# Kernel optimization log

Hardware: AMD Instinct MI355X
Metric: run time of the kernel (lower is better)

## Reference

```python
import jax, jax.numpy as jnp
import numpy as np

N = 6144          # nodes
F_IN = 512        # num_feature
HID = 64          # hidden_dim
C = 40            # num_class
H = 3             # num_heads
ALPHA = 0.2       # leaky relu slope
NEG_INF = -9e15


def gat_layer(x, adj, W, a_src, a_dst):
    # x: [N, f_in], W: [H, f_in, f_out], a_src/a_dst: [H, f_out]
    Wh = jnp.einsum('nf,hfo->hno', x, W)                  # [H, N, f_out]
    e_src = jnp.einsum('hno,ho->hn', Wh, a_src)           # [H, N]
    e_dst = jnp.einsum('hno,ho->hn', Wh, a_dst)           # [H, N]
    e = jax.nn.leaky_relu(e_src[:, :, None] + e_dst[:, None, :], ALPHA)  # [H, N, N]
    scores = jnp.where(adj > 0, e, NEG_INF)               # mask non-edges
    attn = jax.nn.softmax(scores, axis=-1)                # softmax over neighbors
    out = jnp.einsum('hnm,hmo->hno', attn, Wh)            # [H, N, f_out]
    return out.mean(axis=0)                               # average heads -> [N, f_out]


def setup_inputs() -> dict:
    key = jax.random.key(0)
    k = jax.random.split(key, 8)
    feature = jax.random.normal(k[0], (N, F_IN), dtype=jnp.float32)
    adj = (jax.random.uniform(k[1], (N, N)) < 0.01).astype(jnp.float32)
    adj = jnp.maximum(adj, jnp.eye(N, dtype=jnp.float32))
    s1 = 1.0 / np.sqrt(F_IN)
    s2 = 1.0 / np.sqrt(HID)
    W1 = jax.random.normal(k[2], (H, F_IN, HID), dtype=jnp.float32) * s1
    a1_src = jax.random.normal(k[3], (H, HID), dtype=jnp.float32) * s2
    a1_dst = jax.random.normal(k[4], (H, HID), dtype=jnp.float32) * s2
    W2 = jax.random.normal(k[5], (H, HID, C), dtype=jnp.float32) * s2
    a2_src = jax.random.normal(k[6], (H, C), dtype=jnp.float32) * (1.0 / np.sqrt(C))
    a2_dst = jax.random.normal(k[7], (H, C), dtype=jnp.float32) * (1.0 / np.sqrt(C))
    return {"feature": feature, "adj": adj, "W1": W1, "a1_src": a1_src,
            "a1_dst": a1_dst, "W2": W2, "a2_src": a2_src, "a2_dst": a2_dst}


def reference(feature, adj, W1, a1_src, a1_dst, W2, a2_src, a2_dst):
    # eval mode: dropout is identity
    x = jax.nn.relu(gat_layer(feature, adj, W1, a1_src, a1_dst))  # [N, HID]
    x = gat_layer(x, adj, W2, a2_src, a2_dst)                     # [N, C]
    return jax.nn.log_softmax(x, axis=1)
```

## Files before the change

### kernel.cpp

```cpp
#include <hip/hip_runtime.h>
#include <math.h>

#define NN   6144
#define FIN  512
#define HIDN 64
#define NC   40
#define NH   3
#define CAP  128
#define NCHUNK (CAP / 64)
#define LALPHA 0.2f
#define KSPLIT 4
#define PK_LOW  0x3FFFu
#define PK_HIGH 0xFFFFC000u

__device__ __forceinline__ float bf2f(ushort s) {
    return __uint_as_float((unsigned)s << 16);
}
__device__ __forceinline__ ushort f2bf(float f) {
    unsigned u = __float_as_uint(f);
    return (ushort)((u + 0x7FFFu + ((u >> 16) & 1u)) >> 16);
}

__global__ __launch_bounds__(256) void k_csr(const float* __restrict__ adj,
                                             int* __restrict__ nbr,
                                             int* __restrict__ deg) {
    int row  = blockIdx.x * 4 + (threadIdx.x >> 6);
    int lane = threadIdx.x & 63;
    const float* arow = adj + (size_t)row * NN;
    int* nrow = nbr + (size_t)row * CAP;
    int cnt = 0;

    float4 cur[4], nxt[4];
#pragma unroll
    for (int i = 0; i < 4; i++)
        cur[i] = *reinterpret_cast<const float4*>(arow + i * 256 + lane * 4);

#pragma unroll
    for (int g = 0; g < 6; g++) {
        if (g < 5) {
#pragma unroll
            for (int i = 0; i < 4; i++)
                nxt[i] = *reinterpret_cast<const float4*>(arow + (g + 1) * 1024 + i * 256 + lane * 4);
        }
#pragma unroll
        for (int i = 0; i < 4; i++) {
            int base = g * 1024 + i * 256;
            float vv[4] = {cur[i].x, cur[i].y, cur[i].z, cur[i].w};
#pragma unroll
            for (int q = 0; q < 4; q++) {
                bool on = vv[q] > 0.0f;
                unsigned long long mask = __ballot(on);
                if (on) {
                    int pos = cnt + __popcll(mask & ((1ull << lane) - 1ull));
                    if (pos < CAP) nrow[pos] = base + lane * 4 + q;
                }
                cnt += __popcll(mask);
            }
        }
#pragma unroll
        for (int i = 0; i < 4; i++) cur[i] = nxt[i];
    }
    if (lane == 0) deg[row] = cnt < CAP ? cnt : CAP;
}

__global__ __launch_bounds__(256) void k_gemm1(const float* __restrict__ x,
                                               const float* __restrict__ W,
                                               float* __restrict__ Whp) {
    __shared__ float xs[64][68];
    __shared__ float wsh[64][68];
    int h  = blockIdx.y;
    int n0 = blockIdx.x * 64;
    int kz = blockIdx.z;
    int tid = threadIdx.x;
    int og4 = (tid & 15) * 4;
    int mg4 = (tid >> 4) * 4;

    float acc[4][4] = {{0.f}};

    const float* xbase0 = x + (size_t)n0 * FIN;
    const float* wbase0 = W + (size_t)h * FIN * HIDN;

    for (int t = 0; t < 2; t++) {
        int k0 = kz * 128 + t * 64;
#pragma unroll
        for (int i = 0; i < 4; i++) {
            int l = tid + i * 256;
            int r = l >> 4;
            int c = (l & 15) * 4;
            *reinterpret_cast<float4*>(&xs[r][c]) =
                *reinterpret_cast<const float4*>(xbase0 + (size_t)r * FIN + k0 + c);
            *reinterpret_cast<float4*>(&wsh[r][c]) =
                *reinterpret_cast<const float4*>(wbase0 + (size_t)(k0 + r) * HIDN + c);
        }
        __syncthreads();

#pragma unroll 8
        for (int k = 0; k < 64; k += 4) {
            float4 xv[4], wv[4];
            xv[0] = *reinterpret_cast<const float4*>(&xs[mg4 + 0][k]);
            xv[1] = *reinterpret_cast<const float4*>(&xs[mg4 + 1][k]);
            xv[2] = *reinterpret_cast<const float4*>(&xs[mg4 + 2][k]);
            xv[3] = *reinterpret_cast<const float4*>(&xs[mg4 + 3][k]);
            wv[0] = *reinterpret_cast<const float4*>(&wsh[k + 0][og4]);
            wv[1] = *reinterpret_cast<const float4*>(&wsh[k + 1][og4]);
            wv[2] = *reinterpret_cast<const float4*>(&wsh[k + 2][og4]);
            wv[3] = *reinterpret_cast<const float4*>(&wsh[k + 3][og4]);
            const float* xf = reinterpret_cast<const float*>(xv);
            const float* wf = reinterpret_cast<const float*>(wv);
#pragma unroll
            for (int i = 0; i < 4; i++) {
#pragma unroll
                for (int kk = 0; kk < 4; kk++) {
                    float xval = xf[i * 4 + kk];
#pragma unroll
                    for (int j = 0; j < 4; j++)
                        acc[i][j] += xval * wf[kk * 4 + j];
                }
            }
        }
        __syncthreads();
    }

    float* outp = Whp + (((size_t)kz * NH + h) * NN + n0 + mg4) * HIDN + og4;
#pragma unroll
    for (int i = 0; i < 4; i++) {
        float4 v = make_float4(acc[i][0], acc[i][1], acc[i][2], acc[i][3]);
        *reinterpret_cast<float4*>(outp + (size_t)i * HIDN) = v;
    }
}

__global__ __launch_bounds__(256) void k_sum_e1(const float* __restrict__ Whp,
                                                const float* __restrict__ a_src,
                                                const float* __restrict__ a_dst,
                                                ushort* __restrict__ Whb,
                                                float* __restrict__ es,
                                                float* __restrict__ ed) {
    int gw   = blockIdx.x * 4 + (threadIdx.x >> 6);
    int lane = threadIdx.x & 63;
    int h = gw / NN, n = gw % NN;
    size_t idx = ((size_t)h * NN + n) * HIDN + lane;
    size_t stride = (size_t)NH * NN * HIDN;
    float v = Whp[idx] + Whp[idx + stride] + Whp[idx + 2 * stride] + Whp[idx + 3 * stride];
    Whb[idx] = f2bf(v);
    float s = v * a_src[h * HIDN + lane];
    float d = v * a_dst[h * HIDN + lane];
#pragma unroll
    for (int off = 32; off; off >>= 1) {
        s += __shfl_xor(s, off);
        d += __shfl_xor(d, off);
    }
    if (lane == 0) { es[h * NN + n] = s; ed[h * NN + n] = d; }
}

__global__ __launch_bounds__(192) void k_attn1f(const int* __restrict__ nbr,
                                                const int* __restrict__ deg,
                                                const ushort* __restrict__ Whb,
                                                const float* __restrict__ es,
                                                const float* __restrict__ ed,
                                                const float* __restrict__ W2,
                                                const float* __restrict__ a2s,
                                                const float* __restrict__ a2d,
                                                ushort* __restrict__ Wh2b,
                                                float* __restrict__ e2s,
                                                float* __restrict__ e2d) {
    __shared__ unsigned pks[NH][CAP];
    __shared__ float hsum[NH][HIDN];
    int n = blockIdx.x;
    int h = threadIdx.x >> 6;
    int lane = threadIdx.x & 63;
    int d = deg[n];
    const int* nrow = nbr + (size_t)n * CAP;
    float esv = es[h * NN + n];

    float psum = 0.f;
#pragma unroll
    for (int c = 0; c < NCHUNK; c++) {
        int k = c * 64 + lane;
        unsigned u = 0;
        if (k < d) {
            int mm = nrow[k];
            float e = esv + ed[h * NN + mm];
            float s = e > 0.f ? e : LALPHA * e;
            float p = __expf(s);
            u = (__float_as_uint(p) & PK_HIGH) | (unsigned)mm;
            psum += __uint_as_float(u & PK_HIGH);
        }
        pks[h][k] = u;
    }
#pragma unroll
    for (int off = 32; off; off >>= 1) psum += __shfl_xor(psum, off);
    float inv = 1.f / psum;
    __syncthreads();

    const ushort* WhH = Whb + (size_t)h * NN * HIDN + lane;
    float a0 = 0.f, a1 = 0.f, a2 = 0.f, a3 = 0.f;
    int iters = (d + 3) >> 2;
    for (int g = 0; g < iters; g++) {
        uint4 uu = *reinterpret_cast<const uint4*>(&pks[h][g * 4]);
        a0 += __uint_as_float(uu.x & PK_HIGH) * bf2f(WhH[(size_t)(uu.x & PK_LOW) * HIDN]);
        a1 += __uint_as_float(uu.y & PK_HIGH) * bf2f(WhH[(size_t)(uu.y & PK_LOW) * HIDN]);
        a2 += __uint_as_float(uu.z & PK_HIGH) * bf2f(WhH[(size_t)(uu.z & PK_LOW) * HIDN]);
        a3 += __uint_as_float(uu.w & PK_HIGH) * bf2f(WhH[(size_t)(uu.w & PK_LOW) * HIDN]);
    }
    float hacc = ((a0 + a1) + (a2 + a3));
    hsum[h][lane] = hacc * inv;
    __syncthreads();

    float xv = (hsum[0][lane] + hsum[1][lane] + hsum[2][lane]) * (1.f / NH);
    xv = fmaxf(xv, 0.f);

    int c = lane < NC ? lane : NC - 1;
    float acc = 0.f;
#pragma unroll 8
    for (int o = 0; o < HIDN; o++) {
        float xb = __shfl(xv, o);
        float wv = W2[((size_t)h * HIDN + o) * NC + c];
        acc += xb * wv;
    }
    if (lane >= NC) acc = 0.f;

    float s2 = acc * (lane < NC ? a2s[h * NC + lane] : 0.f);
    float d2 = acc * (lane < NC ? a2d[h * NC + lane] : 0.f);
#pragma unroll
    for (int off = 32; off; off >>= 1) {
        s2 += __shfl_xor(s2, off);
        d2 += __shfl_xor(d2, off);
    }
    if (lane < NC) Wh2b[((size_t)h * NN + n) * NC + lane] = f2bf(acc);
    if (lane == 0) { e2s[h * NN + n] = s2; e2d[h * NN + n] = d2; }
}

__global__ __launch_bounds__(192) void k_attn2(const int* __restrict__ nbr,
                                               const int* __restrict__ deg,
                                               const ushort* __restrict__ Wh2b,
                                               const float* __restrict__ es,
                                               const float* __restrict__ ed,
                                               float* __restrict__ out) {
    __shared__ unsigned pks[NH][CAP];
    __shared__ float hsum[NH][HIDN];
    int n = blockIdx.x;
    int h = threadIdx.x >> 6;
    int lane = threadIdx.x & 63;
    int d = deg[n];
    const int* nrow = nbr + (size_t)n * CAP;
    float esv = es[h * NN + n];

    float psum = 0.f;
#pragma unroll
    for (int c = 0; c < NCHUNK; c++) {
        int k = c * 64 + lane;
        unsigned u = 0;
        if (k < d) {
            int mm = nrow[k];
            float e = esv + ed[h * NN + mm];
            float s = e > 0.f ? e : LALPHA * e;
            float p = __expf(s);
            u = (__float_as_uint(p) & PK_HIGH) | (unsigned)mm;
            psum += __uint_as_float(u & PK_HIGH);
        }
        pks[h][k] = u;
    }
#pragma unroll
    for (int off = 32; off; off >>= 1) psum += __shfl_xor(psum, off);
    float inv = 1.f / psum;
    __syncthreads();

    const ushort* W2H = Wh2b + (size_t)h * NN * NC + (lane < NC ? lane : 0);
    float a0 = 0.f, a1 = 0.f, a2 = 0.f, a3 = 0.f;
    int iters = (d + 3) >> 2;
    for (int g = 0; g < iters; g++) {
        uint4 uu = *reinterpret_cast<const uint4*>(&pks[h][g * 4]);
        a0 += __uint_as_float(uu.x & PK_HIGH) * bf2f(W2H[(size_t)(uu.x & PK_LOW) * NC]);
        a1 += __uint_as_float(uu.y & PK_HIGH) * bf2f(W2H[(size_t)(uu.y & PK_LOW) * NC]);
        a2 += __uint_as_float(uu.z & PK_HIGH) * bf2f(W2H[(size_t)(uu.z & PK_LOW) * NC]);
        a3 += __uint_as_float(uu.w & PK_HIGH) * bf2f(W2H[(size_t)(uu.w & PK_LOW) * NC]);
    }
    float hacc = ((a0 + a1) + (a2 + a3));
    if (lane < NC) hsum[h][lane] = hacc * inv;
    __syncthreads();

    if (threadIdx.x < 64) {
        float a = (lane < NC)
            ? (hsum[0][lane] + hsum[1][lane] + hsum[2][lane]) * (1.f / NH)
            : -INFINITY;
        float mx = a;
#pragma unroll
        for (int off = 32; off; off >>= 1) mx = fmaxf(mx, __shfl_xor(mx, off));
        float ex = (lane < NC) ? __expf(a - mx) : 0.f;
        float se = ex;
#pragma unroll
        for (int off = 32; off; off >>= 1) se += __shfl_xor(se, off);
        if (lane < NC) out[(size_t)n * NC + lane] = a - mx - logf(se);
    }
}

extern "C" void kernel_launch(void* const* d_in, const int* in_sizes, int n_in,
                              void* d_out, int out_size, void* d_ws, size_t ws_size,
                              hipStream_t stream) {
    const float* feature = (const float*)d_in[0];
    const float* adj     = (const float*)d_in[1];
    const float* W1      = (const float*)d_in[2];
    const float* a1_src  = (const float*)d_in[3];
    const float* a1_dst  = (const float*)d_in[4];
    const float* W2      = (const float*)d_in[5];
    const float* a2_src  = (const float*)d_in[6];
    const float* a2_dst  = (const float*)d_in[7];
    float* out = (float*)d_out;

    char* ws = (char*)d_ws;
    size_t off = 0;
    int*    nbr = (int*)(ws + off);    off += (size_t)NN * CAP * sizeof(int);
    int*    deg = (int*)(ws + off);    off += (size_t)NN * sizeof(int);
    float*  Whp = (float*)(ws + off);  off += (size_t)KSPLIT * NH * NN * HIDN * sizeof(float);
    ushort* Whb = (ushort*)(ws + off); off += (size_t)NH * NN * HIDN * sizeof(ushort);
    float*  e1s = (float*)(ws + off);  off += (size_t)NH * NN * sizeof(float);
    float*  e1d = (float*)(ws + off);  off += (size_t)NH * NN * sizeof(float);
    ushort* Wh2b= (ushort*)(ws + off); off += (size_t)NH * NN * NC * sizeof(ushort);
    float*  e2s = (float*)(ws + off);  off += (size_t)NH * NN * sizeof(float);
    float*  e2d = (float*)(ws + off);  off += (size_t)NH * NN * sizeof(float);

    k_csr<<<NN / 4, 256, 0, stream>>>(adj, nbr, deg);
    k_gemm1<<<dim3(NN / 64, NH, KSPLIT), 256, 0, stream>>>(feature, W1, Whp);
    k_sum_e1<<<(NH * NN) / 4, 256, 0, stream>>>(Whp, a1_src, a1_dst, Whb, e1s, e1d);
    k_attn1f<<<NN, 192, 0, stream>>>(nbr, deg, Whb, e1s, e1d, W2, a2_src, a2_dst,
                                     Wh2b, e2s, e2d);
    k_attn2<<<NN, 192, 0, stream>>>(nbr, deg, Wh2b, e2s, e2d, out);
}
```

Measured before the change: 103.5 us.

## Split adjacency CSR build into bitmask pass and fused compaction with head sum

```diff
diff --git a/kernel.cpp b/kernel.cpp
--- a/kernel.cpp
+++ b/kernel.cpp
@@ -12,6 +12,11 @@
 #define KSPLIT 4
 #define PK_LOW  0x3FFFu
 #define PK_HIGH 0xFFFFC000u
+#define NGRP   (NN * NN / 256)
+#define BITS_WAVES 8192
+#define CSRB   (NN / 4)
+
+typedef unsigned long long ull;
 
 __device__ __forceinline__ float bf2f(ushort s) {
     return __uint_as_float((unsigned)s << 16);
@@ -21,46 +26,26 @@
     return (ushort)((u + 0x7FFFu + ((u >> 16) & 1u)) >> 16);
 }
 
-__global__ __launch_bounds__(256) void k_csr(const float* __restrict__ adj,
-                                             int* __restrict__ nbr,
-                                             int* __restrict__ deg) {
-    int row  = blockIdx.x * 4 + (threadIdx.x >> 6);
+__global__ __launch_bounds__(256) void k_bits(const float* __restrict__ adj,
+                                              ull* __restrict__ bits) {
+    int gwid = (blockIdx.x * 256 + (int)threadIdx.x) >> 6;
     int lane = threadIdx.x & 63;
-    const float* arow = adj + (size_t)row * NN;
-    int* nrow = nbr + (size_t)row * CAP;
-    int cnt = 0;
-
-    float4 cur[4], nxt[4];
-#pragma unroll
-    for (int i = 0; i < 4; i++)
-        cur[i] = *reinterpret_cast<const float4*>(arow + i * 256 + lane * 4);
-
-#pragma unroll
-    for (int g = 0; g < 6; g++) {
-        if (g < 5) {
-#pragma unroll
-            for (int i = 0; i < 4; i++)
-                nxt[i] = *reinterpret_cast<const float4*>(arow + (g + 1) * 1024 + i * 256 + lane * 4);
-        }
-#pragma unroll
-        for (int i = 0; i < 4; i++) {
-            int base = g * 1024 + i * 256;
-            float vv[4] = {cur[i].x, cur[i].y, cur[i].z, cur[i].w};
-#pragma unroll
-            for (int q = 0; q < 4; q++) {
-                bool on = vv[q] > 0.0f;
-                unsigned long long mask = __ballot(on);
-                if (on) {
-                    int pos = cnt + __popcll(mask & ((1ull << lane) - 1ull));
-                    if (pos < CAP) nrow[pos] = base + lane * 4 + q;
-                }
-                cnt += __popcll(mask);
-            }
-        }
-#pragma unroll
-        for (int i = 0; i < 4; i++) cur[i] = nxt[i];
-    }
-    if (lane == 0) deg[row] = cnt < CAP ? cnt : CAP;
+#pragma unroll 2
+    for (int it = 0; it < NGRP / BITS_WAVES; it++) {
+        size_t grp = (size_t)it * BITS_WAVES + gwid;
+        const float* p = adj + grp * 256 + lane;
+        float a0 = p[0], a1 = p[64], a2 = p[128], a3 = p[192];
+        ull m0 = __ballot(a0 > 0.f);
+        ull m1 = __ballot(a1 > 0.f);
+        ull m2 = __ballot(a2 > 0.f);
+        ull m3 = __ballot(a3 > 0.f);
+        if (lane == 0) {
+            ulonglong2* q = reinterpret_cast<ulonglong2*>(bits + grp * 4);
+            ulonglong2 v0; v0.x = m0; v0.y = m1;
+            ulonglong2 v1; v1.x = m2; v1.y = m3;
+            q[0] = v0; q[1] = v1;
+        }
+    }
 }
 
 __global__ __launch_bounds__(256) void k_gemm1(const float* __restrict__ x,
@@ -76,7 +61,6 @@
     int mg4 = (tid >> 4) * 4;
 
     float acc[4][4] = {{0.f}};
-
     const float* xbase0 = x + (size_t)n0 * FIN;
     const float* wbase0 = W + (size_t)h * FIN * HIDN;
 
@@ -129,14 +113,52 @@
     }
 }
 
-__global__ __launch_bounds__(256) void k_sum_e1(const float* __restrict__ Whp,
-                                                const float* __restrict__ a_src,
-                                                const float* __restrict__ a_dst,
-                                                ushort* __restrict__ Whb,
-                                                float* __restrict__ es,
-                                                float* __restrict__ ed) {
-    int gw   = blockIdx.x * 4 + (threadIdx.x >> 6);
+__global__ __launch_bounds__(256) void k_csr2_sume1(const ull* __restrict__ bits,
+                                                    int* __restrict__ nbr,
+                                                    int* __restrict__ deg,
+                                                    const float* __restrict__ Whp,
+                                                    const float* __restrict__ a_src,
+                                                    const float* __restrict__ a_dst,
+                                                    ushort* __restrict__ Whb,
+                                                    float* __restrict__ es,
+                                                    float* __restrict__ ed) {
     int lane = threadIdx.x & 63;
+    if (blockIdx.x < CSRB) {
+        int row = blockIdx.x * 4 + ((int)threadIdx.x >> 6);
+        const ull* brow = bits + (size_t)row * 96;
+        ull m0 = brow[lane];
+        ull m1 = (lane < 32) ? brow[64 + lane] : 0ull;
+        int c0 = __popcll(m0), c1 = __popcll(m1);
+        int s0 = c0, s1 = c1;
+#pragma unroll
+        for (int off = 1; off < 64; off <<= 1) {
+            int t0 = __shfl_up(s0, off);
+            int t1 = __shfl_up(s1, off);
+            if (lane >= off) { s0 += t0; s1 += t1; }
+        }
+        int total0 = __shfl(s0, 63);
+        int total  = total0 + __shfl(s1, 63);
+        int pre0 = s0 - c0;
+        int pre1 = total0 + (s1 - c1);
+        if (lane == 0) deg[row] = total < CAP ? total : CAP;
+        int* nrow = nbr + (size_t)row * CAP;
+        int base0 = lane * 64;
+        int pos = pre0;
+        while (m0) {
+            int b = __builtin_ctzll(m0); m0 &= m0 - 1;
+            if (pos < CAP) nrow[pos] = base0 + b;
+            pos++;
+        }
+        int base1 = (64 + lane) * 64;
+        pos = pre1;
+        while (m1) {
+            int b = __builtin_ctzll(m1); m1 &= m1 - 1;
+            if (pos < CAP) nrow[pos] = base1 + b;
+            pos++;
+        }
+        return;
+    }
+    int gw = (blockIdx.x - CSRB) * 4 + ((int)threadIdx.x >> 6);
     int h = gw / NN, n = gw % NN;
     size_t idx = ((size_t)h * NN + n) * HIDN + lane;
     size_t stride = (size_t)NH * NN * HIDN;
@@ -309,6 +331,7 @@
 
     char* ws = (char*)d_ws;
     size_t off = 0;
+    ull*    bits = (ull*)(ws + off);   off += (size_t)NGRP * 4 * sizeof(ull);
     int*    nbr = (int*)(ws + off);    off += (size_t)NN * CAP * sizeof(int);
     int*    deg = (int*)(ws + off);    off += (size_t)NN * sizeof(int);
     float*  Whp = (float*)(ws + off);  off += (size_t)KSPLIT * NH * NN * HIDN * sizeof(float);
@@ -319,9 +342,10 @@
     float*  e2s = (float*)(ws + off);  off += (size_t)NH * NN * sizeof(float);
     float*  e2d = (float*)(ws + off);  off += (size_t)NH * NN * sizeof(float);
 
-    k_csr<<<NN / 4, 256, 0, stream>>>(adj, nbr, deg);
+    k_bits<<<2048, 256, 0, stream>>>(adj, bits);
     k_gemm1<<<dim3(NN / 64, NH, KSPLIT), 256, 0, stream>>>(feature, W1, Whp);
-    k_sum_e1<<<(NH * NN) / 4, 256, 0, stream>>>(Whp, a1_src, a1_dst, Whb, e1s, e1d);
+    k_csr2_sume1<<<CSRB + (NH * NN) / 4, 256, 0, stream>>>(bits, nbr, deg, Whp,
+                                                           a1_src, a1_dst, Whb, e1s, e1d);
     k_attn1f<<<NN, 192, 0, stream>>>(nbr, deg, Whb, e1s, e1d, W2, a2_src, a2_dst,
                                      Wh2b, e2s, e2d);
     k_attn2<<<NN, 192, 0, stream>>>(nbr, deg, Wh2b, e2s, e2d, out);
```

After: 106.8 us. 1.03x slower.

## Split CSR row scan across four wavefronts with shared-memory compaction

Applied to the files above, without the earlier changes.

```diff
diff --git a/kernel.cpp b/kernel.cpp
--- a/kernel.cpp
+++ b/kernel.cpp
@@ -13,6 +13,8 @@
 #define PK_LOW  0x3FFFu
 #define PK_HIGH 0xFFFFC000u
 
+typedef unsigned long long ull;
+
 __device__ __forceinline__ float bf2f(ushort s) {
     return __uint_as_float((unsigned)s << 16);
 }
@@ -24,43 +26,39 @@
 __global__ __launch_bounds__(256) void k_csr(const float* __restrict__ adj,
                                              int* __restrict__ nbr,
                                              int* __restrict__ deg) {
-    int row  = blockIdx.x * 4 + (threadIdx.x >> 6);
+    __shared__ int lidx[4][64];
+    __shared__ int wtot[4];
+    int row  = blockIdx.x;
+    int wid  = threadIdx.x >> 6;
     int lane = threadIdx.x & 63;
-    const float* arow = adj + (size_t)row * NN;
-    int* nrow = nbr + (size_t)row * CAP;
+    const float* base = adj + (size_t)row * NN + wid * (NN / 4);
+    ull below = (1ull << lane) - 1ull;
     int cnt = 0;
-
-    float4 cur[4], nxt[4];
-#pragma unroll
-    for (int i = 0; i < 4; i++)
-        cur[i] = *reinterpret_cast<const float4*>(arow + i * 256 + lane * 4);
-
-#pragma unroll
-    for (int g = 0; g < 6; g++) {
-        if (g < 5) {
-#pragma unroll
-            for (int i = 0; i < 4; i++)
-                nxt[i] = *reinterpret_cast<const float4*>(arow + (g + 1) * 1024 + i * 256 + lane * 4);
-        }
-#pragma unroll
-        for (int i = 0; i < 4; i++) {
-            int base = g * 1024 + i * 256;
-            float vv[4] = {cur[i].x, cur[i].y, cur[i].z, cur[i].w};
-#pragma unroll
-            for (int q = 0; q < 4; q++) {
-                bool on = vv[q] > 0.0f;
-                unsigned long long mask = __ballot(on);
-                if (on) {
-                    int pos = cnt + __popcll(mask & ((1ull << lane) - 1ull));
-                    if (pos < CAP) nrow[pos] = base + lane * 4 + q;
-                }
-                cnt += __popcll(mask);
-            }
-        }
-#pragma unroll
-        for (int i = 0; i < 4; i++) cur[i] = nxt[i];
-    }
-    if (lane == 0) deg[row] = cnt < CAP ? cnt : CAP;
+#pragma unroll
+    for (int ch = 0; ch < 6; ch++) {
+        float4 v = *reinterpret_cast<const float4*>(base + ch * 256 + lane * 4);
+        bool h0 = v.x > 0.f, h1 = v.y > 0.f, h2 = v.z > 0.f, h3 = v.w > 0.f;
+        ull b0 = __ballot(h0), b1 = __ballot(h1), b2 = __ballot(h2), b3 = __ballot(h3);
+        int p = cnt + __popcll(b0 & below) + __popcll(b1 & below)
+                    + __popcll(b2 & below) + __popcll(b3 & below);
+        int col = wid * (NN / 4) + ch * 256 + lane * 4;
+        if (h0) { if (p < 64) lidx[wid][p] = col + 0; p++; }
+        if (h1) { if (p < 64) lidx[wid][p] = col + 1; p++; }
+        if (h2) { if (p < 64) lidx[wid][p] = col + 2; p++; }
+        if (h3) { if (p < 64) lidx[wid][p] = col + 3; p++; }
+        cnt += __popcll(b0) + __popcll(b1) + __popcll(b2) + __popcll(b3);
+    }
+    if (lane == 0) wtot[wid] = cnt;
+    __syncthreads();
+    int t0 = wtot[0], t1 = wtot[1], t2 = wtot[2], t3 = wtot[3];
+    int wb = (wid > 0 ? t0 : 0) + (wid > 1 ? t1 : 0) + (wid > 2 ? t2 : 0);
+    int total = t0 + t1 + t2 + t3;
+    if (threadIdx.x == 0) deg[row] = total < CAP ? total : CAP;
+    int myc = wtot[wid] < 64 ? wtot[wid] : 64;
+    if (lane < myc) {
+        int pos = wb + lane;
+        if (pos < CAP) nbr[(size_t)row * CAP + pos] = lidx[wid][lane];
+    }
 }
 
 __global__ __launch_bounds__(256) void k_gemm1(const float* __restrict__ x,
@@ -76,7 +74,6 @@
     int mg4 = (tid >> 4) * 4;
 
     float acc[4][4] = {{0.f}};
-
     const float* xbase0 = x + (size_t)n0 * FIN;
     const float* wbase0 = W + (size_t)h * FIN * HIDN;
 
@@ -319,7 +316,7 @@
     float*  e2s = (float*)(ws + off);  off += (size_t)NH * NN * sizeof(float);
     float*  e2d = (float*)(ws + off);  off += (size_t)NH * NN * sizeof(float);
 
-    k_csr<<<NN / 4, 256, 0, stream>>>(adj, nbr, deg);
+    k_csr<<<NN, 256, 0, stream>>>(adj, nbr, deg);
     k_gemm1<<<dim3(NN / 64, NH, KSPLIT), 256, 0, stream>>>(feature, W1, Whp);
     k_sum_e1<<<(NH * NN) / 4, 256, 0, stream>>>(Whp, a1_src, a1_dst, Whb, e1s, e1d);
     k_attn1f<<<NN, 192, 0, stream>>>(nbr, deg, Whb, e1s, e1d, W2, a2_src, a2_dst,
```

After: 102.0 us. Within noise of the previous version (-1.5%).
